# Kernel optimization log

Measured on AMD Instinct MI355X. Metric: run time of the kernel, lower is better.

Reference implementation:

```python
import jax, jax.numpy as jnp
import numpy as np

B, C, H, W = 4, 64, 96, 96
O = 64          # out_channel
K = 9           # 3x3 kernel positions
PAD = 1


def conv3x3(x, w, b):
    # NCHW 3x3 conv, stride 1, pad 1
    y = jax.lax.conv_general_dilated(
        x, w, window_strides=(1, 1), padding=((PAD, PAD), (PAD, PAD)),
        dimension_numbers=("NCHW", "OIHW", "NCHW"))
    return y + b[None, :, None, None]


def deform_conv3x3(x, offset, w, b):
    """torchvision-style DeformConv2d, 3x3, stride 1, pad 1, 1 offset group.
    x: [B, Cin, H, W]; offset: [B, 2*K, H, W] ordered (dy, dx) per kernel pos.
    """
    Bb, Cin, Hh, Ww = x.shape
    off = offset.reshape(Bb, K, 2, Hh, Ww)
    ky, kx = jnp.meshgrid(jnp.arange(3), jnp.arange(3), indexing="ij")
    ky = ky.reshape(K).astype(x.dtype)
    kx = kx.reshape(K).astype(x.dtype)
    hh = jnp.arange(Hh, dtype=x.dtype)
    ww = jnp.arange(Ww, dtype=x.dtype)
    # sampling coords: p0 + p_k + delta_p  -> [B, K, H, W]
    py = hh[None, None, :, None] - PAD + ky[None, :, None, None] + off[:, :, 0]
    px = ww[None, None, None, :] - PAD + kx[None, :, None, None] + off[:, :, 1]

    y0 = jnp.floor(py).astype(jnp.int32)
    x0 = jnp.floor(px).astype(jnp.int32)
    dy = py - y0.astype(x.dtype)
    dx = px - x0.astype(x.dtype)

    x_flat = x.reshape(Bb, Cin, Hh * Ww)

    def gather(yi, xi, wgt):
        valid = ((yi >= 0) & (yi < Hh) & (xi >= 0) & (xi < Ww)).astype(x.dtype)
        idx = (jnp.clip(yi, 0, Hh - 1) * Ww + jnp.clip(xi, 0, Ww - 1)).reshape(Bb, -1)
        vals = jax.vmap(lambda xf, ix: xf[:, ix])(x_flat, idx)  # [B, Cin, K*H*W]
        return vals * (wgt * valid).reshape(Bb, 1, -1)

    sampled = (gather(y0,     x0,     (1 - dy) * (1 - dx))
             + gather(y0,     x0 + 1, (1 - dy) * dx)
             + gather(y0 + 1, x0,     dy * (1 - dx))
             + gather(y0 + 1, x0 + 1, dy * dx))
    sampled = sampled.reshape(Bb, Cin, K, Hh, Ww)
    out = jnp.einsum("bckhw,ock->bohw", sampled, w.reshape(O, Cin, K))
    return out + b[None, :, None, None]


def setup_inputs() -> dict:
    key = jax.random.key(0)
    ks = jax.random.split(key, 6)
    ref_feat = jax.random.normal(ks[0], (B, C, H, W), dtype=jnp.float32)
    dist_feat = jax.random.normal(ks[1], (B, C, H, W), dtype=jnp.float32)
    offset_w = jax.random.normal(ks[2], (2 * K, C, 3, 3), dtype=jnp.float32) * 0.01
    offset_b = jnp.zeros((2 * K,), dtype=jnp.float32)
    deform_w = jax.random.normal(ks[3], (O, 3 * C, 3, 3), dtype=jnp.float32) * 0.05
    deform_b = jax.random.normal(ks[4], (O,), dtype=jnp.float32) * 0.05
    return {"ref_feat": ref_feat, "dist_feat": dist_feat,
            "offset_w": offset_w, "offset_b": offset_b,
            "deform_w": deform_w, "deform_b": deform_b}


def reference(ref_feat, dist_feat, offset_w, offset_b, deform_w, deform_b):
    offset = conv3x3(ref_feat, offset_w, offset_b)
    diff = (ref_feat - dist_feat) ** 2
    feat_in = jnp.concatenate((ref_feat, dist_feat, diff), axis=1)  # [B, 3C, H, W]
    feat = deform_conv3x3(feat_in, offset, deform_w, deform_b)
    feat = jax.nn.relu(feat)
    return (feat, diff)
```

## Files before the change

### kernel.cpp

```cpp
#include <hip/hip_runtime.h>
#include <hip/hip_bf16.h>

#define Wd    96
#define Hd    96
#define HW    9216
#define Bn    4
#define Cn    64
#define C3    192
#define On    64
#define NPIX  (Bn*HW)
#define NFEAT (Bn*Cn*HW)
#define NWTB  (9*6*4*512)
#define NWTB2 (18*2*64*8)
#define NRB2  (Bn*(HW/16))

#define HR    5
#define HC    21
#define HPITCH 400
#define NPR   (HR*HC)

typedef __attribute__((ext_vector_type(8))) short s8v;
typedef __attribute__((ext_vector_type(4))) unsigned int u4v;
typedef __attribute__((ext_vector_type(4))) float f4v;
typedef __hip_bfloat16 bf16;

__device__ __forceinline__ short f2bfs(float x) {
    return __builtin_bit_cast(short, __float2bfloat16(x));
}
__device__ __forceinline__ float blo(unsigned u) {
    return __builtin_bit_cast(float, u << 16);
}
__device__ __forceinline__ float bhi(unsigned u) {
    return __builtin_bit_cast(float, u & 0xffff0000u);
}
__device__ __forceinline__ unsigned packbf(float lo, float hi) {
    unsigned a = (unsigned)(unsigned short)f2bfs(lo);
    unsigned b = (unsigned)(unsigned short)f2bfs(hi);
    return a | (b << 16);
}

__global__ __launch_bounds__(128) void repack_wts_kernel(
        const float* __restrict__ ref,
        const float* __restrict__ dist,
        unsigned int* __restrict__ packed,
        float* __restrict__ out_diff,
        const float* __restrict__ dw,
        const float* __restrict__ ow,
        bf16* __restrict__ wtb,
        bf16* __restrict__ wtb2) {
    __shared__ unsigned lds[96][17];

    int tid = threadIdx.x;

    if (blockIdx.x >= NRB2) {
        int e = (int)(blockIdx.x - NRB2) * 128 + tid;
        if (e < NWTB) {
            int j = e & 7;
            int L = (e >> 3) & 63;
            int mt = (e >> 9) & 3;
            int rest = e >> 11;
            int kc = rest % 6;
            int tap = rest / 6;
            int o = mt * 16 + (L & 15);
            int c = kc * 32 + (L >> 4) * 8 + j;
            wtb[e] = __float2bfloat16(dw[((size_t)o * C3 + c) * 9 + tap]);
        } else if (e < NWTB + NWTB2) {
            int e2 = e - NWTB;
            int j = e2 & 7;
            int L = (e2 >> 3) & 63;
            int mt = (e2 >> 9) & 1;
            int kc2 = e2 >> 10;
            int v = mt * 16 + (L & 15);
            int k = kc2 * 32 + ((L >> 4) & 3) * 8 + j;
            int c = k & 63;
            int tap = k >> 6;
            float val = (v < 18) ? ow[((size_t)v * Cn + c) * 9 + tap] : 0.f;
            wtb2[e2] = __float2bfloat16(val);
        }
        return;
    }

    int blk = blockIdx.x;
    int b = blk / (HW / 16);
    int pb = (blk - b * (HW / 16)) * 16;
    int pxg = tid & 3;
    int chp = tid >> 2;

    size_t base0 = ((size_t)(b * Cn + 2 * chp)) * HW + pb + pxg * 4;
    size_t base1 = base0 + HW;

    f4v r0 = *(const f4v*)(ref + base0);
    f4v r1 = *(const f4v*)(ref + base1);
    f4v d0 = *(const f4v*)(dist + base0);
    f4v d1 = *(const f4v*)(dist + base1);

    f4v q0 = (r0 - d0) * (r0 - d0);
    f4v q1 = (r1 - d1) * (r1 - d1);
    *(f4v*)(out_diff + base0) = q0;
    *(f4v*)(out_diff + base1) = q1;

#pragma unroll
    for (int j = 0; j < 4; ++j) {
        int p = pxg * 4 + j;
        lds[chp][p]      = packbf(r0[j], r1[j]);
        lds[32 + chp][p] = packbf(d0[j], d1[j]);
        lds[64 + chp][p] = packbf(q0[j], q1[j]);
    }
    __syncthreads();

    unsigned* pko = packed + (size_t)(b * HW + pb) * 96;
#pragma unroll
    for (int k = 0; k < 12; ++k) {
        int i = tid + k * 128;
        int p = i / 96;
        int cp = i - p * 96;
        pko[p * 96 + cp] = lds[cp][p];
    }
}

struct Ctx {
    int o00, o01, o10, o11;
    int l00, l01, l10, l11;
    float W00, W01, W10, W11;
    int inh;
};

__device__ __forceinline__ Ctx mkctx(int t, int y, int x, int xb, float2 o2) {
    Ctx c;
    float py = (float)(y - 1 + t / 3) + o2.x;
    float pxs = (float)(x - 1 + t % 3) + o2.y;
    float fy = floorf(py), fx = floorf(pxs);
    int y0 = (int)fy, x0 = (int)fx;
    int y1 = y0 + 1, x1 = x0 + 1;
    float ay = py - fy, ax = pxs - fx;
    bool vy0 = (unsigned)y0 < (unsigned)Hd;
    bool vy1 = (unsigned)y1 < (unsigned)Hd;
    bool vx0 = (unsigned)x0 < (unsigned)Wd;
    bool vx1 = (unsigned)x1 < (unsigned)Wd;
    c.W00 = (vy0 && vx0) ? (1.f - ay) * (1.f - ax) : 0.f;
    c.W01 = (vy0 && vx1) ? (1.f - ay) * ax : 0.f;
    c.W10 = (vy1 && vx0) ? ay * (1.f - ax) : 0.f;
    c.W11 = (vy1 && vx1) ? ay * ax : 0.f;
    int y0c = min(max(y0, 0), Hd - 1), y1c = min(max(y1, 0), Hd - 1);
    int x0c = min(max(x0, 0), Wd - 1), x1c = min(max(x1, 0), Wd - 1);
    c.o00 = (y0c * Wd + x0c) * (C3 * 2);
    c.o01 = (y0c * Wd + x1c) * (C3 * 2);
    c.o10 = (y1c * Wd + x0c) * (C3 * 2);
    c.o11 = (y1c * Wd + x1c) * (C3 * 2);
    int iy0 = y0c - y + 2, iy1 = y1c - y + 2;
    int ix0 = x0c - xb + 3, ix1 = x1c - xb + 3;
    c.inh = ((unsigned)iy0 < (unsigned)HR) & ((unsigned)iy1 < (unsigned)HR) &
            ((unsigned)ix0 < (unsigned)HC) & ((unsigned)ix1 < (unsigned)HC);
    c.l00 = (iy0 * HC + ix0) * HPITCH;
    c.l01 = (iy0 * HC + ix1) * HPITCH;
    c.l10 = (iy1 * HC + ix0) * HPITCH;
    c.l11 = (iy1 * HC + ix1) * HPITCH;
    return c;
}

__device__ __forceinline__ void bilin_mfma(const s8v* rw, const Ctx& cc,
        const s8v* __restrict__ Ap, int t, int kb, int L, f4v* acc) {
#pragma unroll
    for (int i = 0; i < 3; ++i) {
        int kc = kb + i;
        u4v u00 = __builtin_bit_cast(u4v, rw[0 * 3 + i]);
        u4v u01 = __builtin_bit_cast(u4v, rw[1 * 3 + i]);
        u4v u10 = __builtin_bit_cast(u4v, rw[2 * 3 + i]);
        u4v u11 = __builtin_bit_cast(u4v, rw[3 * 3 + i]);
        u4v bu;
#pragma unroll
        for (int p = 0; p < 4; ++p) {
            float vlo = cc.W00 * blo(u00[p]) + cc.W01 * blo(u01[p])
                      + cc.W10 * blo(u10[p]) + cc.W11 * blo(u11[p]);
            float vhi = cc.W00 * bhi(u00[p]) + cc.W01 * bhi(u01[p])
                      + cc.W10 * bhi(u10[p]) + cc.W11 * bhi(u11[p]);
            bu[p] = packbf(vlo, vhi);
        }
        s8v bfrag = __builtin_bit_cast(s8v, bu);
#pragma unroll
        for (int mt = 0; mt < 4; ++mt) {
            s8v a = Ap[((t * 6 + kc) * 4 + mt) * 64 + L];
            acc[mt] = __builtin_amdgcn_mfma_f32_16x16x32_bf16(a, bfrag, acc[mt], 0, 0, 0);
        }
    }
}

__global__ __launch_bounds__(192) void fused_mfma(
        const bf16* __restrict__ packed,
        const bf16* __restrict__ wtb2,
        const float* __restrict__ ob,
        const bf16* __restrict__ wtb,
        const float* __restrict__ db,
        float* __restrict__ out) {
    __shared__ f4v halo[NPR * (HPITCH / 16)];
    __shared__ float red[2][64 * 17];
    __shared__ float off_lds[16][18];

    int tid = threadIdx.x;
    int L = tid & 63;
    int wv = tid / 64;
    int px = L & 15;
    int lg = L >> 4;
    int blk = blockIdx.x;
    int region = (blk & 7) * 288 + (blk >> 3);
    int p0 = region * 16;
    int b = p0 / HW;
    int pb = p0 - b * HW;
    int yb = pb / Wd;
    int xb = pb - yb * Wd;
    int x = xb + px, y = yb;
    int tbase = wv * 3;

    const char* pkb = (const char*)packed + (size_t)b * HW * (C3 * 2);
    const char* hb = (const char*)halo;

    for (int i = tid; i < NPR * 24; i += 192) {
        int pr = i / 24;
        int ck = i - pr * 24;
        int iy = pr / HC, ix = pr - iy * HC;
        int gy = min(max(yb - 2 + iy, 0), Hd - 1);
        int gx = min(max(xb - 3 + ix, 0), Wd - 1);
        halo[pr * (HPITCH / 16) + ck] =
            *(const f4v*)(pkb + ((size_t)(gy * Wd + gx)) * (C3 * 2) + ck * 16);
    }
    __syncthreads();

    {
        const s8v* Ap = (const s8v*)wtb2;
        f4v acc0 = {0.f, 0.f, 0.f, 0.f};
        f4v acc1 = {0.f, 0.f, 0.f, 0.f};
#pragma unroll
        for (int tt = 0; tt < 3; ++tt) {
            int t = tbase + tt;
            int ty = t / 3, tx = t - ty * 3;
            int yy = y - 1 + ty, xx = x - 1 + tx;
            bool val = (unsigned)yy < (unsigned)Hd && (unsigned)xx < (unsigned)Wd;
            short m = val ? (short)-1 : (short)0;
            int lofs = ((1 + ty) * HC + (px + 2 + tx)) * HPITCH + lg * 16;
#pragma unroll
            for (int kc = 0; kc < 2; ++kc) {
                s8v bfrag = *(const s8v*)(hb + lofs + kc * 64) & m;
                s8v a0 = Ap[((t * 2 + kc) * 2 + 0) * 64 + L];
                s8v a1 = Ap[((t * 2 + kc) * 2 + 1) * 64 + L];
                acc0 = __builtin_amdgcn_mfma_f32_16x16x32_bf16(a0, bfrag, acc0, 0, 0, 0);
                acc1 = __builtin_amdgcn_mfma_f32_16x16x32_bf16(a1, bfrag, acc1, 0, 0, 0);
            }
        }
        if (wv != 0) {
            float* r = red[wv - 1] + L * 9;
#pragma unroll
            for (int i = 0; i < 4; ++i) r[i] = acc0[i];
#pragma unroll
            for (int i = 0; i < 4; ++i) r[4 + i] = acc1[i];
        }
        __syncthreads();
        if (wv == 0) {
            const float* r0 = red[0] + L * 9;
            const float* r1 = red[1] + L * 9;
#pragma unroll
            for (int r = 0; r < 4; ++r) {
                int v = lg * 4 + r;
                off_lds[px][v] = acc0[r] + r0[r] + r1[r] + ob[v];
            }
            if (lg == 0) {
#pragma unroll
                for (int r = 0; r < 2; ++r)
                    off_lds[px][16 + r] = acc1[r] + r0[4 + r] + r1[4 + r] + ob[16 + r];
            }
        }
        __syncthreads();
    }

    const s8v* Ap = (const s8v*)wtb;

    Ctx ctx[3];
    int ok = 1;
#pragma unroll
    for (int tt = 0; tt < 3; ++tt) {
        int t = tbase + tt;
        float2 o2 = {off_lds[px][2 * t], off_lds[px][2 * t + 1]};
        ctx[tt] = mkctx(t, y, x, xb, o2);
        ok &= ctx[tt].inh;
    }

    f4v acc[4];
    acc[0] = acc[1] = acc[2] = acc[3] = (f4v){0.f, 0.f, 0.f, 0.f};

    if (__all(ok)) {
#pragma unroll
        for (int h = 0; h < 6; ++h) {
            int tt = h >> 1;
            int t = tbase + tt;
            int kb = (h & 1) * 3;
            const Ctx cc = ctx[tt];
            s8v rw[12];
#pragma unroll
            for (int i = 0; i < 3; ++i) {
                int co = ((kb + i) * 4 + lg) * 16;
                rw[0 * 3 + i] = *(const s8v*)(hb + cc.l00 + co);
                rw[1 * 3 + i] = *(const s8v*)(hb + cc.l01 + co);
                rw[2 * 3 + i] = *(const s8v*)(hb + cc.l10 + co);
                rw[3 * 3 + i] = *(const s8v*)(hb + cc.l11 + co);
            }
            bilin_mfma(rw, cc, Ap, t, kb, L, acc);
        }
    } else {
#pragma unroll
        for (int h = 0; h < 6; ++h) {
            int tt = h >> 1;
            int t = tbase + tt;
            int kb = (h & 1) * 3;
            const Ctx cc = ctx[tt];
            s8v rw[12];
#pragma unroll
            for (int i = 0; i < 3; ++i) {
                int co = ((kb + i) * 4 + lg) * 16;
                rw[0 * 3 + i] = *(const s8v*)(pkb + cc.o00 + co);
                rw[1 * 3 + i] = *(const s8v*)(pkb + cc.o01 + co);
                rw[2 * 3 + i] = *(const s8v*)(pkb + cc.o10 + co);
                rw[3 * 3 + i] = *(const s8v*)(pkb + cc.o11 + co);
            }
            bilin_mfma(rw, cc, Ap, t, kb, L, acc);
        }
    }

    if (wv != 0) {
        float* r = red[wv - 1] + L * 17;
#pragma unroll
        for (int mt = 0; mt < 4; ++mt)
#pragma unroll
            for (int q = 0; q < 4; ++q)
                r[mt * 4 + q] = acc[mt][q];
    }
    __syncthreads();
    if (wv == 0) {
        const float* r0 = red[0] + L * 17;
        const float* r1 = red[1] + L * 17;
#pragma unroll
        for (int mt = 0; mt < 4; ++mt) {
#pragma unroll
            for (int q = 0; q < 4; ++q) {
                int o = mt * 16 + lg * 4 + q;
                float v = acc[mt][q] + r0[mt * 4 + q] + r1[mt * 4 + q] + db[o];
                out[((size_t)(b * On + o)) * HW + pb + px] = fmaxf(v, 0.f);
            }
        }
    }
}

extern "C" void kernel_launch(void* const* d_in, const int* in_sizes, int n_in,
                              void* d_out, int out_size, void* d_ws, size_t ws_size,
                              hipStream_t stream) {
    const float* ref  = (const float*)d_in[0];
    const float* dist = (const float*)d_in[1];
    const float* ow   = (const float*)d_in[2];
    const float* ob   = (const float*)d_in[3];
    const float* dw   = (const float*)d_in[4];
    const float* db   = (const float*)d_in[5];

    float* out = (float*)d_out;

    bf16* ws_wtb  = (bf16*)d_ws;
    bf16* ws_wtb2 = ws_wtb + NWTB;
    bf16* ws_pk   = ws_wtb2 + NWTB2;

    int wts_blocks = (NWTB + NWTB2 + 127) / 128;
    repack_wts_kernel<<<NRB2 + wts_blocks, 128, 0, stream>>>(
        ref, dist, (unsigned int*)ws_pk, out + NFEAT, dw, ow, ws_wtb, ws_wtb2);
    fused_mfma<<<NPIX / 16, 192, 0, stream>>>(
        ws_pk, ws_wtb2, ob, ws_wtb, db, out);
}
```

Measured before the change: 131.3 us.

## Split deform halo into two channel halves, use packed bilinear math

The LDS halo now holds only half of the 192 packed channels at a time, so its size roughly halves. The kernel loads the first half, runs the deform MFMA over those channel chunks, synchronizes, then reloads the halo with the second half and finishes. The aim is to cut LDS use per block so more blocks fit per CU, at the cost of an extra barrier and two serialized halo loads. The bilinear interpolation is rewritten with 2-wide float vectors so it can map to packed FMA, and the repack kernel moves to 256-thread blocks covering 32 pixels each.

New measurement: 136.9 us. +4.3%, slower.

```diff
diff --git a/kernel.cpp b/kernel.cpp
--- a/kernel.cpp
+++ b/kernel.cpp
@@ -12,16 +12,17 @@
 #define NFEAT (Bn*Cn*HW)
 #define NWTB  (9*6*4*512)
 #define NWTB2 (18*2*64*8)
-#define NRB2  (Bn*(HW/16))
+#define NRB3  (Bn*(HW/32))
 
 #define HR    5
 #define HC    21
-#define HPITCH 400
+#define HPITCH 208
 #define NPR   (HR*HC)
 
 typedef __attribute__((ext_vector_type(8))) short s8v;
 typedef __attribute__((ext_vector_type(4))) unsigned int u4v;
 typedef __attribute__((ext_vector_type(4))) float f4v;
+typedef __attribute__((ext_vector_type(2))) float f2v;
 typedef __hip_bfloat16 bf16;
 
 __device__ __forceinline__ short f2bfs(float x) {
@@ -32,6 +33,12 @@
 }
 __device__ __forceinline__ float bhi(unsigned u) {
     return __builtin_bit_cast(float, u & 0xffff0000u);
+}
+__device__ __forceinline__ f2v up2(unsigned u) {
+    f2v r;
+    r.x = blo(u);
+    r.y = bhi(u);
+    return r;
 }
 __device__ __forceinline__ unsigned packbf(float lo, float hi) {
     unsigned a = (unsigned)(unsigned short)f2bfs(lo);
@@ -39,7 +46,7 @@
     return a | (b << 16);
 }
 
-__global__ __launch_bounds__(128) void repack_wts_kernel(
+__global__ __launch_bounds__(256) void repack_wts_kernel(
         const float* __restrict__ ref,
         const float* __restrict__ dist,
         unsigned int* __restrict__ packed,
@@ -48,12 +55,12 @@
         const float* __restrict__ ow,
         bf16* __restrict__ wtb,
         bf16* __restrict__ wtb2) {
-    __shared__ unsigned lds[96][17];
+    __shared__ unsigned lds[96][33];
 
     int tid = threadIdx.x;
 
-    if (blockIdx.x >= NRB2) {
-        int e = (int)(blockIdx.x - NRB2) * 128 + tid;
+    if (blockIdx.x >= NRB3) {
+        int e = (int)(blockIdx.x - NRB3) * 256 + tid;
         if (e < NWTB) {
             int j = e & 7;
             int L = (e >> 3) & 63;
@@ -81,10 +88,10 @@
     }
 
     int blk = blockIdx.x;
-    int b = blk / (HW / 16);
-    int pb = (blk - b * (HW / 16)) * 16;
-    int pxg = tid & 3;
-    int chp = tid >> 2;
+    int b = blk / (HW / 32);
+    int pb = (blk - b * (HW / 32)) * 32;
+    int pxg = tid & 7;
+    int chp = tid >> 3;
 
     size_t base0 = ((size_t)(b * Cn + 2 * chp)) * HW + pb + pxg * 4;
     size_t base1 = base0 + HW;
@@ -111,7 +118,7 @@
     unsigned* pko = packed + (size_t)(b * HW + pb) * 96;
 #pragma unroll
     for (int k = 0; k < 12; ++k) {
-        int i = tid + k * 128;
+        int i = tid + k * 256;
         int p = i / 96;
         int cp = i - p * 96;
         pko[p * 96 + cp] = lds[cp][p];
@@ -170,11 +177,11 @@
         u4v bu;
 #pragma unroll
         for (int p = 0; p < 4; ++p) {
-            float vlo = cc.W00 * blo(u00[p]) + cc.W01 * blo(u01[p])
-                      + cc.W10 * blo(u10[p]) + cc.W11 * blo(u11[p]);
-            float vhi = cc.W00 * bhi(u00[p]) + cc.W01 * bhi(u01[p])
-                      + cc.W10 * bhi(u10[p]) + cc.W11 * bhi(u11[p]);
-            bu[p] = packbf(vlo, vhi);
+            f2v v = up2(u00[p]) * cc.W00;
+            v += up2(u01[p]) * cc.W01;
+            v += up2(u10[p]) * cc.W10;
+            v += up2(u11[p]) * cc.W11;
+            bu[p] = packbf(v.x, v.y);
         }
         s8v bfrag = __builtin_bit_cast(s8v, bu);
 #pragma unroll
@@ -214,9 +221,10 @@
     const char* pkb = (const char*)packed + (size_t)b * HW * (C3 * 2);
     const char* hb = (const char*)halo;
 
-    for (int i = tid; i < NPR * 24; i += 192) {
-        int pr = i / 24;
-        int ck = i - pr * 24;
+#pragma unroll 1
+    for (int i = tid; i < NPR * 12; i += 192) {
+        int pr = i / 12;
+        int ck = i - pr * 12;
         int iy = pr / HC, ix = pr - iy * HC;
         int gy = min(max(yb - 2 + iy, 0), Hd - 1);
         int gx = min(max(xb - 3 + ix, 0), Wd - 1);
@@ -282,45 +290,85 @@
         ctx[tt] = mkctx(t, y, x, xb, o2);
         ok &= ctx[tt].inh;
     }
+    int fast = __all(ok);
 
     f4v acc[4];
     acc[0] = acc[1] = acc[2] = acc[3] = (f4v){0.f, 0.f, 0.f, 0.f};
 
-    if (__all(ok)) {
-#pragma unroll
-        for (int h = 0; h < 6; ++h) {
-            int tt = h >> 1;
-            int t = tbase + tt;
-            int kb = (h & 1) * 3;
+    if (fast) {
+#pragma unroll
+        for (int tt = 0; tt < 3; ++tt) {
             const Ctx cc = ctx[tt];
             s8v rw[12];
 #pragma unroll
             for (int i = 0; i < 3; ++i) {
-                int co = ((kb + i) * 4 + lg) * 16;
+                int co = (i * 4 + lg) * 16;
                 rw[0 * 3 + i] = *(const s8v*)(hb + cc.l00 + co);
                 rw[1 * 3 + i] = *(const s8v*)(hb + cc.l01 + co);
                 rw[2 * 3 + i] = *(const s8v*)(hb + cc.l10 + co);
                 rw[3 * 3 + i] = *(const s8v*)(hb + cc.l11 + co);
             }
-            bilin_mfma(rw, cc, Ap, t, kb, L, acc);
+            bilin_mfma(rw, cc, Ap, tbase + tt, 0, L, acc);
         }
     } else {
 #pragma unroll
-        for (int h = 0; h < 6; ++h) {
-            int tt = h >> 1;
-            int t = tbase + tt;
-            int kb = (h & 1) * 3;
+        for (int tt = 0; tt < 3; ++tt) {
             const Ctx cc = ctx[tt];
             s8v rw[12];
 #pragma unroll
             for (int i = 0; i < 3; ++i) {
-                int co = ((kb + i) * 4 + lg) * 16;
+                int co = ((0 + i) * 4 + lg) * 16;
                 rw[0 * 3 + i] = *(const s8v*)(pkb + cc.o00 + co);
                 rw[1 * 3 + i] = *(const s8v*)(pkb + cc.o01 + co);
                 rw[2 * 3 + i] = *(const s8v*)(pkb + cc.o10 + co);
                 rw[3 * 3 + i] = *(const s8v*)(pkb + cc.o11 + co);
             }
-            bilin_mfma(rw, cc, Ap, t, kb, L, acc);
+            bilin_mfma(rw, cc, Ap, tbase + tt, 0, L, acc);
+        }
+    }
+    __syncthreads();
+
+#pragma unroll 1
+    for (int i = tid; i < NPR * 12; i += 192) {
+        int pr = i / 12;
+        int ck = i - pr * 12;
+        int iy = pr / HC, ix = pr - iy * HC;
+        int gy = min(max(yb - 2 + iy, 0), Hd - 1);
+        int gx = min(max(xb - 3 + ix, 0), Wd - 1);
+        halo[pr * (HPITCH / 16) + ck] =
+            *(const f4v*)(pkb + ((size_t)(gy * Wd + gx)) * (C3 * 2) + 192 + ck * 16);
+    }
+    __syncthreads();
+
+    if (fast) {
+#pragma unroll
+        for (int tt = 0; tt < 3; ++tt) {
+            const Ctx cc = ctx[tt];
+            s8v rw[12];
+#pragma unroll
+            for (int i = 0; i < 3; ++i) {
+                int co = (i * 4 + lg) * 16;
+                rw[0 * 3 + i] = *(const s8v*)(hb + cc.l00 + co);
+                rw[1 * 3 + i] = *(const s8v*)(hb + cc.l01 + co);
+                rw[2 * 3 + i] = *(const s8v*)(hb + cc.l10 + co);
+                rw[3 * 3 + i] = *(const s8v*)(hb + cc.l11 + co);
+            }
+            bilin_mfma(rw, cc, Ap, tbase + tt, 3, L, acc);
+        }
+    } else {
+#pragma unroll
+        for (int tt = 0; tt < 3; ++tt) {
+            const Ctx cc = ctx[tt];
+            s8v rw[12];
+#pragma unroll
+            for (int i = 0; i < 3; ++i) {
+                int co = ((3 + i) * 4 + lg) * 16;
+                rw[0 * 3 + i] = *(const s8v*)(pkb + cc.o00 + co);
+                rw[1 * 3 + i] = *(const s8v*)(pkb + cc.o01 + co);
+                rw[2 * 3 + i] = *(const s8v*)(pkb + cc.o10 + co);
+                rw[3 * 3 + i] = *(const s8v*)(pkb + cc.o11 + co);
+            }
+            bilin_mfma(rw, cc, Ap, tbase + tt, 3, L, acc);
         }
     }
 
@@ -364,8 +412,8 @@
     bf16* ws_wtb2 = ws_wtb + NWTB;
     bf16* ws_pk   = ws_wtb2 + NWTB2;
 
-    int wts_blocks = (NWTB + NWTB2 + 127) / 128;
-    repack_wts_kernel<<<NRB2 + wts_blocks, 128, 0, stream>>>(
+    int wts_blocks = (NWTB + NWTB2 + 255) / 256;
+    repack_wts_kernel<<<NRB3 + wts_blocks, 256, 0, stream>>>(
         ref, dist, (unsigned int*)ws_pk, out + NFEAT, dw, ow, ws_wtb, ws_wtb2);
     fused_mfma<<<NPIX / 16, 192, 0, stream>>>(
         ws_pk, ws_wtb2, ob, ws_wtb, db, out);
```

## Switch features and weights to fp16 with packed half2 bilinear interpolation

Applied to the files above, without the earlier changes.

Stores the packed features and both weight sets as fp16 instead of bf16, uses the f16 MFMA, and does the bilinear blend with packed half2 multiply/FMA instead of unpacking to fp32 and repacking. This removes the per-element bf16 conversion and repack ALU work in the hot gather loop. The repack kernel also moves to 256-thread blocks covering 32 pixels each, and the halo load loop is kept rolled. fp16 has less range than bf16 and the blend now accumulates in half precision, so accuracy may shift.

Result: faster. 120.7 us (-8.1%).

```diff
diff --git a/kernel.cpp b/kernel.cpp
--- a/kernel.cpp
+++ b/kernel.cpp
@@ -1,5 +1,5 @@
 #include <hip/hip_runtime.h>
-#include <hip/hip_bf16.h>
+#include <hip/hip_fp16.h>
 
 #define Wd    96
 #define Hd    96
@@ -12,7 +12,7 @@
 #define NFEAT (Bn*Cn*HW)
 #define NWTB  (9*6*4*512)
 #define NWTB2 (18*2*64*8)
-#define NRB2  (Bn*(HW/16))
+#define NRB3  (Bn*(HW/32))
 
 #define HR    5
 #define HC    21
@@ -20,40 +20,30 @@
 #define NPR   (HR*HC)
 
 typedef __attribute__((ext_vector_type(8))) short s8v;
+typedef __attribute__((ext_vector_type(8))) _Float16 h8v;
 typedef __attribute__((ext_vector_type(4))) unsigned int u4v;
 typedef __attribute__((ext_vector_type(4))) float f4v;
-typedef __hip_bfloat16 bf16;
-
-__device__ __forceinline__ short f2bfs(float x) {
-    return __builtin_bit_cast(short, __float2bfloat16(x));
-}
-__device__ __forceinline__ float blo(unsigned u) {
-    return __builtin_bit_cast(float, u << 16);
-}
-__device__ __forceinline__ float bhi(unsigned u) {
-    return __builtin_bit_cast(float, u & 0xffff0000u);
-}
-__device__ __forceinline__ unsigned packbf(float lo, float hi) {
-    unsigned a = (unsigned)(unsigned short)f2bfs(lo);
-    unsigned b = (unsigned)(unsigned short)f2bfs(hi);
-    return a | (b << 16);
-}
-
-__global__ __launch_bounds__(128) void repack_wts_kernel(
+
+__device__ __forceinline__ unsigned packh(float lo, float hi) {
+    __half2 h = __floats2half2_rn(lo, hi);
+    return __builtin_bit_cast(unsigned, h);
+}
+
+__global__ __launch_bounds__(256) void repack_wts_kernel(
         const float* __restrict__ ref,
         const float* __restrict__ dist,
         unsigned int* __restrict__ packed,
         float* __restrict__ out_diff,
         const float* __restrict__ dw,
         const float* __restrict__ ow,
-        bf16* __restrict__ wtb,
-        bf16* __restrict__ wtb2) {
-    __shared__ unsigned lds[96][17];
+        __half* __restrict__ wtb,
+        __half* __restrict__ wtb2) {
+    __shared__ unsigned lds[96][33];
 
     int tid = threadIdx.x;
 
-    if (blockIdx.x >= NRB2) {
-        int e = (int)(blockIdx.x - NRB2) * 128 + tid;
+    if (blockIdx.x >= NRB3) {
+        int e = (int)(blockIdx.x - NRB3) * 256 + tid;
         if (e < NWTB) {
             int j = e & 7;
             int L = (e >> 3) & 63;
@@ -63,7 +53,7 @@
             int tap = rest / 6;
             int o = mt * 16 + (L & 15);
             int c = kc * 32 + (L >> 4) * 8 + j;
-            wtb[e] = __float2bfloat16(dw[((size_t)o * C3 + c) * 9 + tap]);
+            wtb[e] = __float2half(dw[((size_t)o * C3 + c) * 9 + tap]);
         } else if (e < NWTB + NWTB2) {
             int e2 = e - NWTB;
             int j = e2 & 7;
@@ -75,16 +65,16 @@
             int c = k & 63;
             int tap = k >> 6;
             float val = (v < 18) ? ow[((size_t)v * Cn + c) * 9 + tap] : 0.f;
-            wtb2[e2] = __float2bfloat16(val);
+            wtb2[e2] = __float2half(val);
         }
         return;
     }
 
     int blk = blockIdx.x;
-    int b = blk / (HW / 16);
-    int pb = (blk - b * (HW / 16)) * 16;
-    int pxg = tid & 3;
-    int chp = tid >> 2;
+    int b = blk / (HW / 32);
+    int pb = (blk - b * (HW / 32)) * 32;
+    int pxg = tid & 7;
+    int chp = tid >> 3;
 
     size_t base0 = ((size_t)(b * Cn + 2 * chp)) * HW + pb + pxg * 4;
     size_t base1 = base0 + HW;
@@ -102,16 +92,16 @@
 #pragma unroll
     for (int j = 0; j < 4; ++j) {
         int p = pxg * 4 + j;
-        lds[chp][p]      = packbf(r0[j], r1[j]);
-        lds[32 + chp][p] = packbf(d0[j], d1[j]);
-        lds[64 + chp][p] = packbf(q0[j], q1[j]);
+        lds[chp][p]      = packh(r0[j], r1[j]);
+        lds[32 + chp][p] = packh(d0[j], d1[j]);
+        lds[64 + chp][p] = packh(q0[j], q1[j]);
     }
     __syncthreads();
 
     unsigned* pko = packed + (size_t)(b * HW + pb) * 96;
 #pragma unroll
     for (int k = 0; k < 12; ++k) {
-        int i = tid + k * 128;
+        int i = tid + k * 256;
         int p = i / 96;
         int cp = i - p * 96;
         pko[p * 96 + cp] = lds[cp][p];
@@ -158,8 +148,16 @@
     return c;
 }
 
+__device__ __forceinline__ __half2 uh2(unsigned u) {
+    return __builtin_bit_cast(__half2, u);
+}
+
 __device__ __forceinline__ void bilin_mfma(const s8v* rw, const Ctx& cc,
         const s8v* __restrict__ Ap, int t, int kb, int L, f4v* acc) {
+    __half2 w00 = __float2half2_rn(cc.W00);
+    __half2 w01 = __float2half2_rn(cc.W01);
+    __half2 w10 = __float2half2_rn(cc.W10);
+    __half2 w11 = __float2half2_rn(cc.W11);
 #pragma unroll
     for (int i = 0; i < 3; ++i) {
         int kc = kb + i;
@@ -170,26 +168,26 @@
         u4v bu;
 #pragma unroll
         for (int p = 0; p < 4; ++p) {
-            float vlo = cc.W00 * blo(u00[p]) + cc.W01 * blo(u01[p])
-                      + cc.W10 * blo(u10[p]) + cc.W11 * blo(u11[p]);
-            float vhi = cc.W00 * bhi(u00[p]) + cc.W01 * bhi(u01[p])
-                      + cc.W10 * bhi(u10[p]) + cc.W11 * bhi(u11[p]);
-            bu[p] = packbf(vlo, vhi);
-        }
-        s8v bfrag = __builtin_bit_cast(s8v, bu);
+            __half2 v = __hmul2(uh2(u00[p]), w00);
+            v = __hfma2(uh2(u01[p]), w01, v);
+            v = __hfma2(uh2(u10[p]), w10, v);
+            v = __hfma2(uh2(u11[p]), w11, v);
+            bu[p] = __builtin_bit_cast(unsigned, v);
+        }
+        h8v bfrag = __builtin_bit_cast(h8v, bu);
 #pragma unroll
         for (int mt = 0; mt < 4; ++mt) {
-            s8v a = Ap[((t * 6 + kc) * 4 + mt) * 64 + L];
-            acc[mt] = __builtin_amdgcn_mfma_f32_16x16x32_bf16(a, bfrag, acc[mt], 0, 0, 0);
+            h8v a = __builtin_bit_cast(h8v, Ap[((t * 6 + kc) * 4 + mt) * 64 + L]);
+            acc[mt] = __builtin_amdgcn_mfma_f32_16x16x32_f16(a, bfrag, acc[mt], 0, 0, 0);
         }
     }
 }
 
 __global__ __launch_bounds__(192) void fused_mfma(
-        const bf16* __restrict__ packed,
-        const bf16* __restrict__ wtb2,
+        const __half* __restrict__ packed,
+        const __half* __restrict__ wtb2,
         const float* __restrict__ ob,
-        const bf16* __restrict__ wtb,
+        const __half* __restrict__ wtb,
         const float* __restrict__ db,
         float* __restrict__ out) {
     __shared__ f4v halo[NPR * (HPITCH / 16)];
@@ -214,6 +212,7 @@
     const char* pkb = (const char*)packed + (size_t)b * HW * (C3 * 2);
     const char* hb = (const char*)halo;
 
+#pragma unroll 1
     for (int i = tid; i < NPR * 24; i += 192) {
         int pr = i / 24;
         int ck = i - pr * 24;
@@ -239,11 +238,12 @@
             int lofs = ((1 + ty) * HC + (px + 2 + tx)) * HPITCH + lg * 16;
 #pragma unroll
             for (int kc = 0; kc < 2; ++kc) {
-                s8v bfrag = *(const s8v*)(hb + lofs + kc * 64) & m;
-                s8v a0 = Ap[((t * 2 + kc) * 2 + 0) * 64 + L];
-                s8v a1 = Ap[((t * 2 + kc) * 2 + 1) * 64 + L];
-                acc0 = __builtin_amdgcn_mfma_f32_16x16x32_bf16(a0, bfrag, acc0, 0, 0, 0);
-                acc1 = __builtin_amdgcn_mfma_f32_16x16x32_bf16(a1, bfrag, acc1, 0, 0, 0);
+                s8v braw = *(const s8v*)(hb + lofs + kc * 64) & m;
+                h8v bfrag = __builtin_bit_cast(h8v, braw);
+                h8v a0 = __builtin_bit_cast(h8v, Ap[((t * 2 + kc) * 2 + 0) * 64 + L]);
+                h8v a1 = __builtin_bit_cast(h8v, Ap[((t * 2 + kc) * 2 + 1) * 64 + L]);
+                acc0 = __builtin_amdgcn_mfma_f32_16x16x32_f16(a0, bfrag, acc0, 0, 0, 0);
+                acc1 = __builtin_amdgcn_mfma_f32_16x16x32_f16(a1, bfrag, acc1, 0, 0, 0);
             }
         }
         if (wv != 0) {
@@ -360,12 +360,12 @@
 
     float* out = (float*)d_out;
 
-    bf16* ws_wtb  = (bf16*)d_ws;
-    bf16* ws_wtb2 = ws_wtb + NWTB;
-    bf16* ws_pk   = ws_wtb2 + NWTB2;
-
-    int wts_blocks = (NWTB + NWTB2 + 127) / 128;
-    repack_wts_kernel<<<NRB2 + wts_blocks, 128, 0, stream>>>(
+    __half* ws_wtb  = (__half*)d_ws;
+    __half* ws_wtb2 = ws_wtb + NWTB;
+    __half* ws_pk   = ws_wtb2 + NWTB2;
+
+    int wts_blocks = (NWTB + NWTB2 + 255) / 256;
+    repack_wts_kernel<<<NRB3 + wts_blocks, 256, 0, stream>>>(
         ref, dist, (unsigned int*)ws_pk, out + NFEAT, dw, ow, ws_wtb, ws_wtb2);
     fused_mfma<<<NPIX / 16, 192, 0, stream>>>(
         ws_pk, ws_wtb2, ob, ws_wtb, db, out);
```
